# Kernel optimization log

Hardware: AMD Instinct MI355X
Metric: run time of the kernel (lower is better)

Reference implementation:

```python
import jax, jax.numpy as jnp
import numpy as np

BETA = float(np.exp(-1.0 / 10.0))   # tau = 10.0
THRESHOLD = 15.0
SLOPE = 25.0                        # snntorch fast_sigmoid default slope

B = 2097152


def spike(x):
    # Heaviside forward (surrogate grad only matters in bwd module)
    return (x > 0).astype(x.dtype)


def lif_step(cur, mem):
    # snntorch Leaky, reset_mechanism='zero':
    #   reset = H(mem_prev - threshold)  (detached)
    #   base  = beta * mem_prev + cur
    #   mem   = base * (1 - reset)
    #   spk   = H(mem - threshold)
    reset = jax.lax.stop_gradient((mem > THRESHOLD).astype(mem.dtype))
    new_mem = (BETA * mem + cur) * (1.0 - reset)
    spk = spike(new_mem - THRESHOLD)
    return spk, new_mem


def setup_inputs() -> dict:
    key = jax.random.key(0)
    kx, k1, k2, k3 = jax.random.split(key, 4)
    x = jax.random.normal(kx, (B, 2), dtype=jnp.float32) * 10.0  # scaled so some neurons cross threshold=15
    mem1 = jnp.zeros((B, 2), dtype=jnp.float32)
    mem2 = jnp.zeros((B, 3), dtype=jnp.float32)
    mem3 = jnp.zeros((B, 2), dtype=jnp.float32)
    # nn.Linear weights: [out_features, in_features], bias=False
    W1 = jax.random.normal(k1, (2, 2), dtype=jnp.float32)
    W2 = jax.random.normal(k2, (3, 2), dtype=jnp.float32)
    W3 = jax.random.normal(k3, (2, 3), dtype=jnp.float32)
    return {"x": x, "mem1": mem1, "mem2": mem2, "mem3": mem3,
            "W1": W1, "W2": W2, "W3": W3}


def reference(x, mem1, mem2, mem3, W1, W2, W3):
    cur1 = x @ W1.T                       # [B, 2]
    spk1, mem1 = lif_step(cur1, mem1)
    cur2 = spk1 @ W2.T                    # [B, 3]
    spk2, mem2 = lif_step(cur2, mem2)
    cur3 = spk2 @ W3.T                    # [B, 2]
    spk3, mem3 = lif_step(cur3, mem3)
    return (spk3, mem1, mem2, mem3)
```

## Files before the change

kernel.cpp:

```cpp
#include <hip/hip_runtime.h>


#define BETA 0.90483741803595952f
#define THR  15.0f

__device__ __forceinline__ void lif(float cur, float mem_prev, float& nm, float& spk) {
    float base = __fadd_rn(__fmul_rn(BETA, mem_prev), cur);
    nm  = (mem_prev > THR) ? 0.0f : base;
    spk = (nm > THR) ? 1.0f : 0.0f;
}

struct Wts {
    float w1_00, w1_01, w1_10, w1_11;
    float w2_00, w2_01, w2_10, w2_11, w2_20, w2_21;
    float w3_00, w3_01, w3_02, w3_10, w3_11, w3_12;
};

__device__ __forceinline__ void snn_row(const Wts& w,
                                        float x0, float x1,
                                        const float m1[2], const float m2[3], const float m3[2],
                                        float s3[2], float m1o[2], float m2o[3], float m3o[2]) {
    float cur1_0 = __fadd_rn(__fmul_rn(x0, w.w1_00), __fmul_rn(x1, w.w1_01));
    float cur1_1 = __fadd_rn(__fmul_rn(x0, w.w1_10), __fmul_rn(x1, w.w1_11));
    float s1_0, s1_1;
    lif(cur1_0, m1[0], m1o[0], s1_0);
    lif(cur1_1, m1[1], m1o[1], s1_1);

    float cur2_0 = __fadd_rn(__fmul_rn(s1_0, w.w2_00), __fmul_rn(s1_1, w.w2_01));
    float cur2_1 = __fadd_rn(__fmul_rn(s1_0, w.w2_10), __fmul_rn(s1_1, w.w2_11));
    float cur2_2 = __fadd_rn(__fmul_rn(s1_0, w.w2_20), __fmul_rn(s1_1, w.w2_21));
    float s2_0, s2_1, s2_2;
    lif(cur2_0, m2[0], m2o[0], s2_0);
    lif(cur2_1, m2[1], m2o[1], s2_1);
    lif(cur2_2, m2[2], m2o[2], s2_2);

    float cur3_0 = __fadd_rn(__fadd_rn(__fmul_rn(s2_0, w.w3_00), __fmul_rn(s2_1, w.w3_01)),
                             __fmul_rn(s2_2, w.w3_02));
    float cur3_1 = __fadd_rn(__fadd_rn(__fmul_rn(s2_0, w.w3_10), __fmul_rn(s2_1, w.w3_11)),
                             __fmul_rn(s2_2, w.w3_12));
    lif(cur3_0, m3[0], m3o[0], s3[0]);
    lif(cur3_1, m3[1], m3o[1], s3[1]);
}

__global__ __launch_bounds__(256) void snn_kernel(
    const float* __restrict__ x,
    const float* __restrict__ mem1,
    const float* __restrict__ mem2,
    const float* __restrict__ mem3,
    const float* __restrict__ W1, const float* __restrict__ W2, const float* __restrict__ W3,
    float* __restrict__ out,
    int B, long long out_n)
{
    const long long t = (long long)blockIdx.x * blockDim.x + threadIdx.x;
    const long long r0 = t * 4;
    if (r0 >= B) return;

    Wts w;
    w.w1_00 = W1[0]; w.w1_01 = W1[1]; w.w1_10 = W1[2]; w.w1_11 = W1[3];
    w.w2_00 = W2[0]; w.w2_01 = W2[1]; w.w2_10 = W2[2];
    w.w2_11 = W2[3]; w.w2_20 = W2[4]; w.w2_21 = W2[5];
    w.w3_00 = W3[0]; w.w3_01 = W3[1]; w.w3_02 = W3[2];
    w.w3_10 = W3[3]; w.w3_11 = W3[4]; w.w3_12 = W3[5];

    const long long Bl = B;
    const long long out_n4 = out_n >> 2;

    if (r0 + 3 < Bl) {
        const float4* x4  = (const float4*)x;
        const float4* m14 = (const float4*)mem1;
        const float4* m24 = (const float4*)mem2;
        const float4* m34 = (const float4*)mem3;

        float4 xv0 = x4[t * 2 + 0], xv1 = x4[t * 2 + 1];
        float4 a0  = m14[t * 2 + 0], a1 = m14[t * 2 + 1];
        float4 b0  = m24[t * 3 + 0], b1 = m24[t * 3 + 1], b2 = m24[t * 3 + 2];
        float4 c0  = m34[t * 2 + 0], c1 = m34[t * 2 + 1];

        float xr[4][2] = {{xv0.x, xv0.y}, {xv0.z, xv0.w}, {xv1.x, xv1.y}, {xv1.z, xv1.w}};
        float m1[4][2] = {{a0.x, a0.y}, {a0.z, a0.w}, {a1.x, a1.y}, {a1.z, a1.w}};
        float m2[4][3] = {{b0.x, b0.y, b0.z}, {b0.w, b1.x, b1.y},
                          {b1.z, b1.w, b2.x}, {b2.y, b2.z, b2.w}};
        float m3[4][2] = {{c0.x, c0.y}, {c0.z, c0.w}, {c1.x, c1.y}, {c1.z, c1.w}};

        float s3o[4][2], m1o[4][2], m2o[4][3], m3o[4][2];
#pragma unroll
        for (int r = 0; r < 4; ++r)
            snn_row(w, xr[r][0], xr[r][1], m1[r], m2[r], m3[r],
                    s3o[r], m1o[r], m2o[r], m3o[r]);

        float4* o4 = (float4*)out;
        long long f;
        f = t * 2;
        if (f + 1 < out_n4) {
            o4[f + 0] = make_float4(s3o[0][0], s3o[0][1], s3o[1][0], s3o[1][1]);
            o4[f + 1] = make_float4(s3o[2][0], s3o[2][1], s3o[3][0], s3o[3][1]);
        }
        f = (2 * Bl >> 2) + t * 2;
        if (f + 1 < out_n4) {
            o4[f + 0] = make_float4(m1o[0][0], m1o[0][1], m1o[1][0], m1o[1][1]);
            o4[f + 1] = make_float4(m1o[2][0], m1o[2][1], m1o[3][0], m1o[3][1]);
        }
        f = (4 * Bl >> 2) + t * 3;
        if (f + 2 < out_n4) {
            o4[f + 0] = make_float4(m2o[0][0], m2o[0][1], m2o[0][2], m2o[1][0]);
            o4[f + 1] = make_float4(m2o[1][1], m2o[1][2], m2o[2][0], m2o[2][1]);
            o4[f + 2] = make_float4(m2o[2][2], m2o[3][0], m2o[3][1], m2o[3][2]);
        }
        if (((7 * Bl) & 3) == 0) {
            f = (7 * Bl >> 2) + t * 2;
            if (f + 1 < out_n4) {
                o4[f + 0] = make_float4(m3o[0][0], m3o[0][1], m3o[1][0], m3o[1][1]);
                o4[f + 1] = make_float4(m3o[2][0], m3o[2][1], m3o[3][0], m3o[3][1]);
            }
        } else {
            long long i = 7 * Bl + 2 * r0;
            if (i + 7 < out_n) {
#pragma unroll
                for (int r = 0; r < 4; ++r) { out[i + 2*r] = m3o[r][0]; out[i + 2*r + 1] = m3o[r][1]; }
            }
        }
    } else {
        for (long long rr = r0; rr < Bl; ++rr) {
            float m1[2] = {mem1[2*rr], mem1[2*rr+1]};
            float m2[3] = {mem2[3*rr], mem2[3*rr+1], mem2[3*rr+2]};
            float m3[2] = {mem3[2*rr], mem3[2*rr+1]};
            float s3[2], m1o[2], m2o[3], m3o[2];
            snn_row(w, x[2*rr], x[2*rr+1], m1, m2, m3, s3, m1o, m2o, m3o);
            long long i;
            i = 2*rr;           if (i+1 < out_n) { out[i] = s3[0];  out[i+1] = s3[1]; }
            i = 2*Bl + 2*rr;    if (i+1 < out_n) { out[i] = m1o[0]; out[i+1] = m1o[1]; }
            i = 4*Bl + 3*rr;    if (i+2 < out_n) { out[i] = m2o[0]; out[i+1] = m2o[1]; out[i+2] = m2o[2]; }
            i = 7*Bl + 2*rr;    if (i+1 < out_n) { out[i] = m3o[0]; out[i+1] = m3o[1]; }
        }
    }
}

extern "C" void kernel_launch(void* const* d_in, const int* in_sizes, int n_in,
                              void* d_out, int out_size, void* d_ws, size_t ws_size,
                              hipStream_t stream) {
    const float* x    = (const float*)d_in[0];
    const float* mem1 = (const float*)d_in[1];
    const float* mem2 = (const float*)d_in[2];
    const float* mem3 = (const float*)d_in[3];
    const float* W1   = (const float*)d_in[4];
    const float* W2   = (const float*)d_in[5];
    const float* W3   = (const float*)d_in[6];
    float* out        = (float*)d_out;

    const int B = in_sizes[0] / 2;
    const int threads = (B + 3) / 4;
    const int block = 256;
    const int grid = (threads + block - 1) / block;

    snn_kernel<<<grid, block, 0, stream>>>(x, mem1, mem2, mem3, W1, W2, W3,
                                           out, B, (long long)out_size);
}
```

Before: 147.9 us.

## Use nontemporal vector loads/stores with grid-stride loop and 32-bit indexing

Replaces the one-task-per-thread launch with a fixed 512-block grid-stride loop. All streaming float4 loads and stores now go through nontemporal builtins so they bypass cache retention. Index math is narrowed to 32-bit unsigned. This targets cache pollution and per-thread setup and address overhead, but a fixed grid of 512 blocks may leave fewer waves in flight to hide memory latency on a many-CU device.

Measured after the change: 149.5 us. About the same (+1.1%).

```diff
diff --git a/kernel.cpp b/kernel.cpp
--- a/kernel.cpp
+++ b/kernel.cpp
@@ -3,6 +3,8 @@
 
 #define BETA 0.90483741803595952f
 #define THR  15.0f
+
+typedef float f32x4 __attribute__((ext_vector_type(4)));
 
 __device__ __forceinline__ void lif(float cur, float mem_prev, float& nm, float& spk) {
     float base = __fadd_rn(__fmul_rn(BETA, mem_prev), cur);
@@ -42,6 +44,14 @@
     lif(cur3_1, m3[1], m3o[1], s3[1]);
 }
 
+__device__ __forceinline__ f32x4 ntload4(const f32x4* p) {
+    return __builtin_nontemporal_load(p);
+}
+__device__ __forceinline__ void ntstore4(f32x4* p, float a, float b, float c, float d) {
+    f32x4 v = {a, b, c, d};
+    __builtin_nontemporal_store(v, p);
+}
+
 __global__ __launch_bounds__(256) void snn_kernel(
     const float* __restrict__ x,
     const float* __restrict__ mem1,
@@ -49,12 +59,8 @@
     const float* __restrict__ mem3,
     const float* __restrict__ W1, const float* __restrict__ W2, const float* __restrict__ W3,
     float* __restrict__ out,
-    int B, long long out_n)
+    unsigned int B, unsigned int out_n)
 {
-    const long long t = (long long)blockIdx.x * blockDim.x + threadIdx.x;
-    const long long r0 = t * 4;
-    if (r0 >= B) return;
-
     Wts w;
     w.w1_00 = W1[0]; w.w1_01 = W1[1]; w.w1_10 = W1[2]; w.w1_11 = W1[3];
     w.w2_00 = W2[0]; w.w2_01 = W2[1]; w.w2_10 = W2[2];
@@ -62,75 +68,77 @@
     w.w3_00 = W3[0]; w.w3_01 = W3[1]; w.w3_02 = W3[2];
     w.w3_10 = W3[3]; w.w3_11 = W3[4]; w.w3_12 = W3[5];
 
-    const long long Bl = B;
-    const long long out_n4 = out_n >> 2;
+    const unsigned int ntasks = (B + 3u) >> 2;
+    const unsigned int stride = gridDim.x * blockDim.x;
+    const unsigned int out_n4 = out_n >> 2;
+    const unsigned int o_m1_f4 = (2u * B) >> 2;
+    const unsigned int o_m2_f4 = (4u * B) >> 2;
+    const unsigned int o_m3_f4 = (7u * B) >> 2;
+    const bool aligned = ((B & 3u) == 0u);
 
-    if (r0 + 3 < Bl) {
-        const float4* x4  = (const float4*)x;
-        const float4* m14 = (const float4*)mem1;
-        const float4* m24 = (const float4*)mem2;
-        const float4* m34 = (const float4*)mem3;
+    const f32x4* x4  = (const f32x4*)x;
+    const f32x4* m14 = (const f32x4*)mem1;
+    const f32x4* m24 = (const f32x4*)mem2;
+    const f32x4* m34 = (const f32x4*)mem3;
+    f32x4* o4 = (f32x4*)out;
 
-        float4 xv0 = x4[t * 2 + 0], xv1 = x4[t * 2 + 1];
-        float4 a0  = m14[t * 2 + 0], a1 = m14[t * 2 + 1];
-        float4 b0  = m24[t * 3 + 0], b1 = m24[t * 3 + 1], b2 = m24[t * 3 + 2];
-        float4 c0  = m34[t * 2 + 0], c1 = m34[t * 2 + 1];
+    for (unsigned int t = blockIdx.x * blockDim.x + threadIdx.x; t < ntasks; t += stride) {
+        const unsigned int r0 = t << 2;
 
-        float xr[4][2] = {{xv0.x, xv0.y}, {xv0.z, xv0.w}, {xv1.x, xv1.y}, {xv1.z, xv1.w}};
-        float m1[4][2] = {{a0.x, a0.y}, {a0.z, a0.w}, {a1.x, a1.y}, {a1.z, a1.w}};
-        float m2[4][3] = {{b0.x, b0.y, b0.z}, {b0.w, b1.x, b1.y},
-                          {b1.z, b1.w, b2.x}, {b2.y, b2.z, b2.w}};
-        float m3[4][2] = {{c0.x, c0.y}, {c0.z, c0.w}, {c1.x, c1.y}, {c1.z, c1.w}};
+        if (aligned && r0 + 3u < B) {
+            f32x4 xv0 = ntload4(&x4[t * 2 + 0]), xv1 = ntload4(&x4[t * 2 + 1]);
+            f32x4 a0  = ntload4(&m14[t * 2 + 0]), a1 = ntload4(&m14[t * 2 + 1]);
+            f32x4 b0  = ntload4(&m24[t * 3 + 0]), b1 = ntload4(&m24[t * 3 + 1]),
+                  b2  = ntload4(&m24[t * 3 + 2]);
+            f32x4 c0  = ntload4(&m34[t * 2 + 0]), c1 = ntload4(&m34[t * 2 + 1]);
 
-        float s3o[4][2], m1o[4][2], m2o[4][3], m3o[4][2];
+            float xr[4][2] = {{xv0.x, xv0.y}, {xv0.z, xv0.w}, {xv1.x, xv1.y}, {xv1.z, xv1.w}};
+            float m1[4][2] = {{a0.x, a0.y}, {a0.z, a0.w}, {a1.x, a1.y}, {a1.z, a1.w}};
+            float m2[4][3] = {{b0.x, b0.y, b0.z}, {b0.w, b1.x, b1.y},
+                              {b1.z, b1.w, b2.x}, {b2.y, b2.z, b2.w}};
+            float m3[4][2] = {{c0.x, c0.y}, {c0.z, c0.w}, {c1.x, c1.y}, {c1.z, c1.w}};
+
+            float s3o[4][2], m1o[4][2], m2o[4][3], m3o[4][2];
 #pragma unroll
-        for (int r = 0; r < 4; ++r)
-            snn_row(w, xr[r][0], xr[r][1], m1[r], m2[r], m3[r],
-                    s3o[r], m1o[r], m2o[r], m3o[r]);
+            for (int r = 0; r < 4; ++r)
+                snn_row(w, xr[r][0], xr[r][1], m1[r], m2[r], m3[r],
+                        s3o[r], m1o[r], m2o[r], m3o[r]);
 
-        float4* o4 = (float4*)out;
-        long long f;
-        f = t * 2;
-        if (f + 1 < out_n4) {
-            o4[f + 0] = make_float4(s3o[0][0], s3o[0][1], s3o[1][0], s3o[1][1]);
-            o4[f + 1] = make_float4(s3o[2][0], s3o[2][1], s3o[3][0], s3o[3][1]);
-        }
-        f = (2 * Bl >> 2) + t * 2;
-        if (f + 1 < out_n4) {
-            o4[f + 0] = make_float4(m1o[0][0], m1o[0][1], m1o[1][0], m1o[1][1]);
-            o4[f + 1] = make_float4(m1o[2][0], m1o[2][1], m1o[3][0], m1o[3][1]);
-        }
-        f = (4 * Bl >> 2) + t * 3;
-        if (f + 2 < out_n4) {
-            o4[f + 0] = make_float4(m2o[0][0], m2o[0][1], m2o[0][2], m2o[1][0]);
-            o4[f + 1] = make_float4(m2o[1][1], m2o[1][2], m2o[2][0], m2o[2][1]);
-            o4[f + 2] = make_float4(m2o[2][2], m2o[3][0], m2o[3][1], m2o[3][2]);
-        }
-        if (((7 * Bl) & 3) == 0) {
-            f = (7 * Bl >> 2) + t * 2;
+            unsigned int f;
+            f = t * 2;
             if (f + 1 < out_n4) {
-                o4[f + 0] = make_float4(m3o[0][0], m3o[0][1], m3o[1][0], m3o[1][1]);
-                o4[f + 1] = make_float4(m3o[2][0], m3o[2][1], m3o[3][0], m3o[3][1]);
+                ntstore4(&o4[f + 0], s3o[0][0], s3o[0][1], s3o[1][0], s3o[1][1]);
+                ntstore4(&o4[f + 1], s3o[2][0], s3o[2][1], s3o[3][0], s3o[3][1]);
+            }
+            f = o_m1_f4 + t * 2;
+            if (f + 1 < out_n4) {
+                ntstore4(&o4[f + 0], m1o[0][0], m1o[0][1], m1o[1][0], m1o[1][1]);
+                ntstore4(&o4[f + 1], m1o[2][0], m1o[2][1], m1o[3][0], m1o[3][1]);
+            }
+            f = o_m2_f4 + t * 3;
+            if (f + 2 < out_n4) {
+                ntstore4(&o4[f + 0], m2o[0][0], m2o[0][1], m2o[0][2], m2o[1][0]);
+                ntstore4(&o4[f + 1], m2o[1][1], m2o[1][2], m2o[2][0], m2o[2][1]);
+                ntstore4(&o4[f + 2], m2o[2][2], m2o[3][0], m2o[3][1], m2o[3][2]);
+            }
+            f = o_m3_f4 + t * 2;
+            if (f + 1 < out_n4) {
+                ntstore4(&o4[f + 0], m3o[0][0], m3o[0][1], m3o[1][0], m3o[1][1]);
+                ntstore4(&o4[f + 1], m3o[2][0], m3o[2][1], m3o[3][0], m3o[3][1]);
             }
         } else {
-            long long i = 7 * Bl + 2 * r0;
-            if (i + 7 < out_n) {
-#pragma unroll
-                for (int r = 0; r < 4; ++r) { out[i + 2*r] = m3o[r][0]; out[i + 2*r + 1] = m3o[r][1]; }
+            for (unsigned int rr = r0; rr < B; ++rr) {
+                float m1[2] = {mem1[2*rr], mem1[2*rr+1]};
+                float m2[3] = {mem2[3*rr], mem2[3*rr+1], mem2[3*rr+2]};
+                float m3[2] = {mem3[2*rr], mem3[2*rr+1]};
+                float s3[2], m1o[2], m2o[3], m3o[2];
+                snn_row(w, x[2*rr], x[2*rr+1], m1, m2, m3, s3, m1o, m2o, m3o);
+                unsigned int i;
+                i = 2*rr;          if (i+1 < out_n) { out[i] = s3[0];  out[i+1] = s3[1]; }
+                i = 2*B + 2*rr;    if (i+1 < out_n) { out[i] = m1o[0]; out[i+1] = m1o[1]; }
+                i = 4*B + 3*rr;    if (i+2 < out_n) { out[i] = m2o[0]; out[i+1] = m2o[1]; out[i+2] = m2o[2]; }
+                i = 7*B + 2*rr;    if (i+1 < out_n) { out[i] = m3o[0]; out[i+1] = m3o[1]; }
             }
-        }
-    } else {
-        for (long long rr = r0; rr < Bl; ++rr) {
-            float m1[2] = {mem1[2*rr], mem1[2*rr+1]};
-            float m2[3] = {mem2[3*rr], mem2[3*rr+1], mem2[3*rr+2]};
-            float m3[2] = {mem3[2*rr], mem3[2*rr+1]};
-            float s3[2], m1o[2], m2o[3], m3o[2];
-            snn_row(w, x[2*rr], x[2*rr+1], m1, m2, m3, s3, m1o, m2o, m3o);
-            long long i;
-            i = 2*rr;           if (i+1 < out_n) { out[i] = s3[0];  out[i+1] = s3[1]; }
-            i = 2*Bl + 2*rr;    if (i+1 < out_n) { out[i] = m1o[0]; out[i+1] = m1o[1]; }
-            i = 4*Bl + 3*rr;    if (i+2 < out_n) { out[i] = m2o[0]; out[i+1] = m2o[1]; out[i+2] = m2o[2]; }
-            i = 7*Bl + 2*rr;    if (i+1 < out_n) { out[i] = m3o[0]; out[i+1] = m3o[1]; }
         }
     }
 }
@@ -147,11 +155,10 @@
     const float* W3   = (const float*)d_in[6];
     float* out        = (float*)d_out;
 
-    const int B = in_sizes[0] / 2;
-    const int threads = (B + 3) / 4;
+    const unsigned int B = (unsigned int)(in_sizes[0] / 2);
     const int block = 256;
-    const int grid = (threads + block - 1) / block;
+    const int grid = 512;
 
     snn_kernel<<<grid, block, 0, stream>>>(x, mem1, mem2, mem3, W1, W2, W3,
-                                           out, B, (long long)out_size);
+                                           out, B, (unsigned int)out_size);
 }
```
